# Performance work log

Hardware: AMD Instinct MI355X
Metric: run time of the kernel (lower is better)

## Reference

```python
import jax, jax.numpy as jnp
import numpy as np

D_MODEL = 2048
N_HEADS = 32
N_KV = 8
D_K = D_MODEL // N_HEADS  # 64
N_REP = N_HEADS // N_KV   # 4


def setup_inputs() -> dict:
    key = jax.random.key(0)
    ks = jax.random.split(key, 5)
    B, T = 2, 2048
    s = 0.02
    return {
        "x": jax.random.normal(ks[0], (B, T, D_MODEL), dtype=jnp.float32),
        "Wq": jax.random.normal(ks[1], (D_MODEL, D_MODEL), dtype=jnp.float32) * s,
        "Wk": jax.random.normal(ks[2], (N_KV * D_K, D_MODEL), dtype=jnp.float32) * s,
        "Wv": jax.random.normal(ks[3], (N_KV * D_K, D_MODEL), dtype=jnp.float32) * s,
        "Wo": jax.random.normal(ks[4], (D_MODEL, D_MODEL), dtype=jnp.float32) * s,
    }


def reference(x, Wq, Wk, Wv, Wo):
    B, T, C = x.shape
    # projections (torch Linear: x @ W.T)
    Q = (x @ Wq.T).reshape(B, T, N_KV, N_REP, D_K)  # group query heads by kv group
    K = (x @ Wk.T).reshape(B, T, N_KV, D_K)
    V = (x @ Wv.T).reshape(B, T, N_KV, D_K)
    scale = 1.0 / jnp.sqrt(jnp.asarray(D_K, dtype=x.dtype))
    # scores: (B, n_kv, n_rep, T, T) == repeated-KV scores without materializing repeats
    scores = jnp.einsum('btgrd,bsgd->bgrts', Q, K) * scale
    causal_mask = jnp.triu(jnp.ones((T, T), dtype=bool), k=1)
    scores = jnp.where(causal_mask, -jnp.inf, scores)
    attn = jax.nn.softmax(scores, axis=-1)
    out = jnp.einsum('bgrts,bsgd->btgrd', attn, V).reshape(B, T, C)
    return out @ Wo.T
```

## Files before the change

### kernel.cpp

```cpp
#include <hip/hip_runtime.h>
#include <hip/hip_bf16.h>

typedef __attribute__((ext_vector_type(8))) short bf16x8;
typedef __attribute__((ext_vector_type(4))) float floatx4;

constexpr int D_MODEL = 2048;
constexpr int N_HEADS = 32;
constexpr int N_KV    = 8;
constexpr int B_      = 2;
constexpr int T_      = 2048;
constexpr int BT      = B_ * T_;
constexpr int NQKV    = 3072;

constexpr float Q_SCALE = 0.18033688011112042f;

__device__ __forceinline__ unsigned short f2bf(float f) {
    __hip_bfloat16 h = __float2bfloat16(f);
    return *reinterpret_cast<unsigned short*>(&h);
}

__device__ __forceinline__ unsigned bfpack_rn(float a, float b) {
    unsigned ba = __builtin_bit_cast(unsigned, a);
    unsigned bb = __builtin_bit_cast(unsigned, b);
    return ((ba + 0x8000u) >> 16) | ((bb + 0x8000u) & 0xFFFF0000u);
}

__device__ __forceinline__ void gll16(const void* g, void* l) {
    typedef const __attribute__((address_space(1))) unsigned int* gp_t;
    typedef __attribute__((address_space(3))) unsigned int* lp_t;
    __builtin_amdgcn_global_load_lds((gp_t)g, (lp_t)l, 16, 0, 0);
}

__global__ __launch_bounds__(256) void cvt_all(
        const float* __restrict__ x,  const float* __restrict__ wq,
        const float* __restrict__ wk, const float* __restrict__ wv,
        unsigned short* __restrict__ dst) {
    size_t i4 = (size_t)blockIdx.x * 256 + threadIdx.x;
    size_t e = i4 * 4;
    const float* src; size_t off;
    if (e < 8388608)        { src = x;  off = 0; }
    else if (e < 12582912)  { src = wq; off = 8388608; }
    else if (e < 13631488)  { src = wk; off = 12582912; }
    else                    { src = wv; off = 13631488; }
    float4 f = *reinterpret_cast<const float4*>(src + (e - off));
    unsigned short u[4] = {f2bf(f.x), f2bf(f.y), f2bf(f.z), f2bf(f.w)};
    reinterpret_cast<uint2*>(dst)[i4] = *reinterpret_cast<const uint2*>(u);
}

__global__ __launch_bounds__(256) void cvt_bf16(
        const float* __restrict__ src, unsigned short* __restrict__ dst, int n4) {
    int i = blockIdx.x * 256 + threadIdx.x;
    if (i < n4) {
        float4 f = reinterpret_cast<const float4*>(src)[i];
        unsigned short u[4] = {f2bf(f.x), f2bf(f.y), f2bf(f.z), f2bf(f.w)};
        reinterpret_cast<uint2*>(dst)[i] = *reinterpret_cast<const uint2*>(u);
    }
}

template<bool C_F32, bool SCALEQ>
__global__ __launch_bounds__(256) void gemm128(
        const unsigned short* __restrict__ A,
        const unsigned short* __restrict__ Bb,
        void* __restrict__ Cp,
        int M, int N, int K) {
    __shared__ unsigned short As[128 * 64];
    __shared__ unsigned short Bs[128 * 64];
    const int t = threadIdx.x;
    const int wave = t >> 6, lane = t & 63;
    const int l16 = lane & 15, quad = lane >> 4;
    const int wm = (wave & 1) * 64, wn = (wave >> 1) * 64;
    const int mtile = blockIdx.y * 128, ntile = blockIdx.x * 128;

    floatx4 acc[4][4] = {};

    for (int k0 = 0; k0 < K; k0 += 64) {
        __syncthreads();
#pragma unroll
        for (int c = 0; c < 4; c++) {
            int s = (c * 4 + wave) * 64 + lane;
            int row = s >> 3, k8 = (s & 7) ^ (row & 7);
            gll16(&A[(size_t)(mtile + row) * K + k0 + k8 * 8], &As[(c * 4 + wave) * 512]);
            gll16(&Bb[(size_t)(ntile + row) * K + k0 + k8 * 8], &Bs[(c * 4 + wave) * 512]);
        }
        __syncthreads();
#pragma unroll
        for (int kc = 0; kc < 2; kc++) {
            bf16x8 af[4], bfr[4];
#pragma unroll
            for (int i = 0; i < 4; i++) {
                int arow = wm + i * 16 + l16;
                af[i] = *reinterpret_cast<const bf16x8*>(
                    &As[(arow * 8 + ((kc * 4 + quad) ^ (arow & 7))) * 8]);
                int brow = wn + i * 16 + l16;
                bfr[i] = *reinterpret_cast<const bf16x8*>(
                    &Bs[(brow * 8 + ((kc * 4 + quad) ^ (brow & 7))) * 8]);
            }
#pragma unroll
            for (int i = 0; i < 4; i++)
#pragma unroll
                for (int jn = 0; jn < 4; jn++)
                    acc[i][jn] = __builtin_amdgcn_mfma_f32_16x16x32_bf16(
                        af[i], bfr[jn], acc[i][jn], 0, 0, 0);
        }
    }
    float cscale = (SCALEQ && ntile < 2048) ? Q_SCALE : 1.0f;
#pragma unroll
    for (int i = 0; i < 4; i++)
#pragma unroll
        for (int jn = 0; jn < 4; jn++)
#pragma unroll
            for (int r = 0; r < 4; r++) {
                int row = mtile + wm + i * 16 + quad * 4 + r;
                int col = ntile + wn + jn * 16 + l16;
                if constexpr (C_F32)
                    ((float*)Cp)[(size_t)row * N + col] = acc[i][jn][r];
                else
                    ((unsigned short*)Cp)[(size_t)row * N + col] =
                        f2bf(acc[i][jn][r] * cscale);
            }
}

__global__ __launch_bounds__(256) void vtrans(
        const unsigned short* __restrict__ QKV,
        unsigned short* __restrict__ Vt) {
    __shared__ unsigned short Ts[64][72];
    const int tb = blockIdx.x * 64;
    const int bg = blockIdx.y;
    const int b = bg >> 3, g = bg & 7;
    const int t = threadIdx.x;
#pragma unroll
    for (int it = 0; it < 2; it++) {
        int row = (t >> 3) + it * 32;
        int sl = t & 7;
        *reinterpret_cast<uint4*>(&Ts[row][sl * 8]) =
            *reinterpret_cast<const uint4*>(
                &QKV[(size_t)(b * T_ + tb + row) * NQKV + 2560 + g * 64 + sl * 8]);
    }
    __syncthreads();
#pragma unroll
    for (int it = 0; it < 2; it++) {
        int d = (t >> 3) + it * 32;
        int ks = t & 7;
        unsigned short u[8];
#pragma unroll
        for (int j = 0; j < 8; j++) u[j] = Ts[ks * 8 + j][d];
        *reinterpret_cast<uint4*>(&Vt[((size_t)bg * 64 + d) * T_ + tb + ks * 8]) =
            *reinterpret_cast<const uint4*>(u);
    }
}

__global__ __launch_bounds__(512, 4) void attn7(
        const unsigned short* __restrict__ QKV,
        const unsigned short* __restrict__ Vt,
        unsigned short* __restrict__ O) {
    __shared__ unsigned short Ks[64 * 64];
    __shared__ unsigned short Vs[64 * 64];
    __shared__ unsigned short Ps[8][16 * 72];
    const int j  = blockIdx.x;
    const int bh = blockIdx.y;
    const int b = bh >> 5, h = bh & 31;
    const int g = h >> 2;
    const int t = threadIdx.x, wave = t >> 6, lane = t & 63;
    const int l16 = lane & 15, quad = lane >> 4;

    bf16x8 ones;
#pragma unroll
    for (int i = 0; i < 8; i++) ones[i] = (short)0x3F80;

    const int srow = t >> 3;
    const int sk8  = (t & 7) ^ (srow & 7);
    const unsigned short* kbase =
        QKV + (size_t)(b * T_ + srow) * NQKV + 2048 + g * 64 + sk8 * 8;
    const unsigned short* vbase =
        Vt + ((size_t)(b * 8 + g) * 64 + srow) * T_ + sk8 * 8;
    unsigned short* kdst = &Ks[wave * 512];
    unsigned short* vdst = &Vs[wave * 512];

    for (int pp = 0; pp < 2; pp++) {
        const int qtl = pp ? (15 - j) : j;
        const int q0  = qtl * 128;
        const int qlo = q0 + wave * 16;

        const unsigned short* qptr =
            QKV + (size_t)(b * T_ + qlo + l16) * NQKV + h * 64;
        bf16x8 qf0 = *reinterpret_cast<const bf16x8*>(qptr + quad * 8);
        bf16x8 qf1 = *reinterpret_cast<const bf16x8*>(qptr + 32 + quad * 8);

        floatx4 o[4] = {};
        floatx4 lacc = {};

        const unsigned short* kp = kbase;
        const unsigned short* vp = vbase;

        const int nkt = 2 * qtl + 2;
        for (int kt = 0; kt < nkt; kt++) {
            const int kb = kt * 64;
            __syncthreads();
            gll16(kp, kdst);
            gll16(vp, vdst);
            kp += 64 * NQKV;
            vp += 64;
            __syncthreads();

            if (kb > qlo + 15) continue;
            const bool needmask = (kb + 63 > qlo);

#pragma unroll
            for (int km = 0; km < 4; km++) {
                int krow = km * 16 + l16;
                bf16x8 k0 = *reinterpret_cast<const bf16x8*>(
                    &Ks[(krow * 8 + (quad ^ (krow & 7))) * 8]);
                bf16x8 k1 = *reinterpret_cast<const bf16x8*>(
                    &Ks[(krow * 8 + ((4 + quad) ^ (krow & 7))) * 8]);
                floatx4 z = {};
                __builtin_amdgcn_s_setprio(1);
                z = __builtin_amdgcn_mfma_f32_16x16x32_bf16(k0, qf0, z, 0, 0, 0);
                z = __builtin_amdgcn_mfma_f32_16x16x32_bf16(k1, qf1, z, 0, 0, 0);
                __builtin_amdgcn_s_setprio(0);
                float p[4];
#pragma unroll
                for (int r = 0; r < 4; r++)
                    p[r] = __builtin_amdgcn_exp2f(z[r]);
                if (needmask) {
                    int qq = qlo + l16;
#pragma unroll
                    for (int r = 0; r < 4; r++)
                        if ((kb + km * 16 + quad * 4 + r) > qq) p[r] = 0.f;
                }
                uint2 w;
                w.x = bfpack_rn(p[0], p[1]);
                w.y = bfpack_rn(p[2], p[3]);
                *reinterpret_cast<uint2*>(
                    &Ps[wave][l16 * 72 + km * 16 + quad * 4]) = w;
            }

            bf16x8 pf[2];
            __builtin_amdgcn_s_setprio(1);
#pragma unroll
            for (int ks = 0; ks < 2; ks++)
                pf[ks] = *reinterpret_cast<const bf16x8*>(
                    &Ps[wave][l16 * 72 + ks * 32 + quad * 8]);
            lacc = __builtin_amdgcn_mfma_f32_16x16x32_bf16(pf[0], ones, lacc, 0, 0, 0);
            lacc = __builtin_amdgcn_mfma_f32_16x16x32_bf16(pf[1], ones, lacc, 0, 0, 0);
#pragma unroll
            for (int dt = 0; dt < 4; dt++) {
                int vrow = dt * 16 + l16;
                bf16x8 v0 = *reinterpret_cast<const bf16x8*>(
                    &Vs[(vrow * 8 + (quad ^ (vrow & 7))) * 8]);
                bf16x8 v1 = *reinterpret_cast<const bf16x8*>(
                    &Vs[(vrow * 8 + ((4 + quad) ^ (vrow & 7))) * 8]);
                o[dt] = __builtin_amdgcn_mfma_f32_16x16x32_bf16(pf[0], v0, o[dt], 0, 0, 0);
                o[dt] = __builtin_amdgcn_mfma_f32_16x16x32_bf16(pf[1], v1, o[dt], 0, 0, 0);
            }
            __builtin_amdgcn_s_setprio(0);
        }

#pragma unroll
        for (int r = 0; r < 4; r++) {
            float inv = 1.0f / lacc[r];
            int row = b * T_ + qlo + quad * 4 + r;
#pragma unroll
            for (int dt = 0; dt < 4; dt++)
                O[(size_t)row * D_MODEL + h * 64 + dt * 16 + l16] =
                    f2bf(o[dt][r] * inv);
        }
    }
}

extern "C" void kernel_launch(void* const* d_in, const int* in_sizes, int n_in,
                              void* d_out, int out_size, void* d_ws, size_t ws_size,
                              hipStream_t stream) {
    const float* x  = (const float*)d_in[0];
    const float* Wq = (const float*)d_in[1];
    const float* Wk = (const float*)d_in[2];
    const float* Wv = (const float*)d_in[3];
    const float* Wo = (const float*)d_in[4];

    unsigned short* xb   = (unsigned short*)d_ws;
    unsigned short* Wqkv = xb + (size_t)BT * D_MODEL;
    unsigned short* QKVo = Wqkv + (size_t)NQKV * D_MODEL;
    unsigned short* Vt   = QKVo + (size_t)BT * NQKV;
    unsigned short* Aw   = xb;
    unsigned short* Wob  = Wqkv;

    dim3 blk(256);
    cvt_all<<<dim3(14336), blk, 0, stream>>>(x, Wq, Wk, Wv, xb);
    gemm128<false, true><<<dim3(NQKV / 128, BT / 128), blk, 0, stream>>>(
        xb, Wqkv, QKVo, BT, NQKV, D_MODEL);
    cvt_bf16<<<dim3(D_MODEL * D_MODEL / 4 / 256), blk, 0, stream>>>(
        Wo, Wob, D_MODEL * D_MODEL / 4);
    vtrans<<<dim3(T_ / 64, B_ * N_KV), blk, 0, stream>>>(QKVo, Vt);
    attn7<<<dim3(8, B_ * N_HEADS), dim3(512), 0, stream>>>(QKVo, Vt, Aw);
    gemm128<true, false><<<dim3(D_MODEL / 128, BT / 128), blk, 0, stream>>>(
        Aw, Wob, d_out, BT, D_MODEL, D_MODEL);
}
```

Baseline: 272.8 us.

## Fuse V transpose into QKV GEMM epilogue and remap blocks across XCDs

Removes the separate vtrans kernel: the QKV GEMM epilogue now writes V columns directly into the transposed Vt buffer as well as the row-major output. It also remaps block IDs so that consecutive tiles land on the same XCD chunk, which is meant to improve L2 locality on the 8-XCD MI355X. The fused transposed stores are scattered 2-byte writes with stride T, so they may be poorly coalesced. The block remap assumes the grid size is divisible by 8.

New measurement: 287.8 us. +5.5%, slower.

```diff
diff --git a/kernel.cpp b/kernel.cpp
--- a/kernel.cpp
+++ b/kernel.cpp
@@ -57,11 +57,12 @@
     }
 }
 
-template<bool C_F32, bool SCALEQ>
+template<bool C_F32, bool SCALEQ, bool FUSEV>
 __global__ __launch_bounds__(256) void gemm128(
         const unsigned short* __restrict__ A,
         const unsigned short* __restrict__ Bb,
         void* __restrict__ Cp,
+        unsigned short* __restrict__ Vtp,
         int M, int N, int K) {
     __shared__ unsigned short As[128 * 64];
     __shared__ unsigned short Bs[128 * 64];
@@ -69,7 +70,12 @@
     const int wave = t >> 6, lane = t & 63;
     const int l16 = lane & 15, quad = lane >> 4;
     const int wm = (wave & 1) * 64, wn = (wave >> 1) * 64;
-    const int mtile = blockIdx.y * 128, ntile = blockIdx.x * 128;
+
+    const int gx = gridDim.x;
+    int bid = blockIdx.y * gx + blockIdx.x;
+    const int cpx = (gx * gridDim.y) >> 3;
+    bid = (bid & 7) * cpx + (bid >> 3);
+    const int mtile = (bid / gx) * 128, ntile = (bid % gx) * 128;
 
     floatx4 acc[4][4] = {};
 
@@ -107,46 +113,26 @@
 #pragma unroll
     for (int i = 0; i < 4; i++)
 #pragma unroll
-        for (int jn = 0; jn < 4; jn++)
+        for (int jn = 0; jn < 4; jn++) {
+            int col = ntile + wn + jn * 16 + l16;
 #pragma unroll
             for (int r = 0; r < 4; r++) {
                 int row = mtile + wm + i * 16 + quad * 4 + r;
-                int col = ntile + wn + jn * 16 + l16;
-                if constexpr (C_F32)
+                if constexpr (C_F32) {
                     ((float*)Cp)[(size_t)row * N + col] = acc[i][jn][r];
-                else
-                    ((unsigned short*)Cp)[(size_t)row * N + col] =
-                        f2bf(acc[i][jn][r] * cscale);
-            }
-}
-
-__global__ __launch_bounds__(256) void vtrans(
-        const unsigned short* __restrict__ QKV,
-        unsigned short* __restrict__ Vt) {
-    __shared__ unsigned short Ts[64][72];
-    const int tb = blockIdx.x * 64;
-    const int bg = blockIdx.y;
-    const int b = bg >> 3, g = bg & 7;
-    const int t = threadIdx.x;
-#pragma unroll
-    for (int it = 0; it < 2; it++) {
-        int row = (t >> 3) + it * 32;
-        int sl = t & 7;
-        *reinterpret_cast<uint4*>(&Ts[row][sl * 8]) =
-            *reinterpret_cast<const uint4*>(
-                &QKV[(size_t)(b * T_ + tb + row) * NQKV + 2560 + g * 64 + sl * 8]);
-    }
-    __syncthreads();
-#pragma unroll
-    for (int it = 0; it < 2; it++) {
-        int d = (t >> 3) + it * 32;
-        int ks = t & 7;
-        unsigned short u[8];
-#pragma unroll
-        for (int j = 0; j < 8; j++) u[j] = Ts[ks * 8 + j][d];
-        *reinterpret_cast<uint4*>(&Vt[((size_t)bg * 64 + d) * T_ + tb + ks * 8]) =
-            *reinterpret_cast<const uint4*>(u);
-    }
+                } else {
+                    unsigned short v = f2bf(acc[i][jn][r] * cscale);
+                    ((unsigned short*)Cp)[(size_t)row * N + col] = v;
+                    if constexpr (FUSEV)
+                        if (col >= 2560) {
+                            int d = col - 2560;
+                            int gg = d >> 6, dd = d & 63;
+                            int bb = row >> 11, tok = row & 2047;
+                            Vtp[(((size_t)bb * 8 + gg) * 64 + dd) * T_ + tok] = v;
+                        }
+                }
+            }
+        }
 }
 
 __global__ __launch_bounds__(512, 4) void attn7(
@@ -285,12 +271,11 @@
 
     dim3 blk(256);
     cvt_all<<<dim3(14336), blk, 0, stream>>>(x, Wq, Wk, Wv, xb);
-    gemm128<false, true><<<dim3(NQKV / 128, BT / 128), blk, 0, stream>>>(
-        xb, Wqkv, QKVo, BT, NQKV, D_MODEL);
+    gemm128<false, true, true><<<dim3(NQKV / 128, BT / 128), blk, 0, stream>>>(
+        xb, Wqkv, QKVo, Vt, BT, NQKV, D_MODEL);
     cvt_bf16<<<dim3(D_MODEL * D_MODEL / 4 / 256), blk, 0, stream>>>(
         Wo, Wob, D_MODEL * D_MODEL / 4);
-    vtrans<<<dim3(T_ / 64, B_ * N_KV), blk, 0, stream>>>(QKVo, Vt);
     attn7<<<dim3(8, B_ * N_HEADS), dim3(512), 0, stream>>>(QKVo, Vt, Aw);
-    gemm128<true, false><<<dim3(D_MODEL / 128, BT / 128), blk, 0, stream>>>(
-        Aw, Wob, d_out, BT, D_MODEL, D_MODEL);
-}
+    gemm128<true, false, false><<<dim3(D_MODEL / 128, BT / 128), blk, 0, stream>>>(
+        Aw, Wob, d_out, nullptr, BT, D_MODEL, D_MODEL);
+}
```
